# Performance work log

Hardware: AMD Instinct MI355X
Metric: run time of the kernel (lower is better)

The kernel has to match this reference:

```python
import jax, jax.numpy as jnp
import numpy as np

B, S, D, H = 4, 2048, 1024, 16
HD = D // H


def setup_inputs() -> dict:
    key = jax.random.key(0)
    ks = jax.random.split(key, 5)
    s_in = 1.0 / np.sqrt(D)
    return {
        "x": jax.random.normal(ks[0], (B, S, D), dtype=jnp.float32),
        "W_attn": jax.random.uniform(ks[1], (D, 3 * D), dtype=jnp.float32, minval=-s_in, maxval=s_in),
        "b_attn": jax.random.uniform(ks[2], (3 * D,), dtype=jnp.float32, minval=-s_in, maxval=s_in),
        "W_proj": jax.random.uniform(ks[3], (D, D), dtype=jnp.float32, minval=-s_in, maxval=s_in),
        "b_proj": jax.random.uniform(ks[4], (D,), dtype=jnp.float32, minval=-s_in, maxval=s_in),
    }


def reference(x, W_attn, b_attn, W_proj, b_proj):
    b, s, d = x.shape
    qkv = x @ W_attn + b_attn                      # [B,S,3D]
    q, k, v = jnp.split(qkv, 3, axis=-1)
    # [B,H,S,HD]
    q = q.reshape(b, s, H, HD).transpose(0, 2, 1, 3)
    k = k.reshape(b, s, H, HD).transpose(0, 2, 1, 3)
    v = v.reshape(b, s, H, HD).transpose(0, 2, 1, 3)
    scale = 1.0 / np.sqrt(HD)
    att = jnp.einsum("bhqd,bhkd->bhqk", q, k) * scale
    causal = jnp.tril(jnp.ones((s, s), dtype=bool))
    att = jnp.where(causal[None, None], att, -jnp.inf)
    att = jax.nn.softmax(att, axis=-1)
    y = jnp.einsum("bhqk,bhkd->bhqd", att, v)      # [B,H,S,HD]
    y = y.transpose(0, 2, 1, 3).reshape(b, s, d)
    return y @ W_proj + b_proj
```

## Files before the change

kernel.cpp:

```cpp
#include <hip/hip_runtime.h>

#define B_  4
#define S_  2048
#define D_  1024
#define H_  16
#define HD_ 64
#define BS_ (B_*S_)

typedef _Float16 f16;
typedef _Float16 f16_8 __attribute__((ext_vector_type(8)));
typedef _Float16 f16_4 __attribute__((ext_vector_type(4)));
typedef float    f32_4 __attribute__((ext_vector_type(4)));
typedef unsigned int u32;

#define MFMA32(a,b,c) __builtin_amdgcn_mfma_f32_16x16x32_f16(a, b, c, 0, 0, 0)
#define MFMA16(a,b,c) __builtin_amdgcn_mfma_f32_16x16x16f16(a, b, c, 0, 0, 0)
#define NEG_INF (-__builtin_inff())

__device__ inline void gl_lds16(const f16* g, f16* lds_base, int chunk_base) {
    __builtin_amdgcn_global_load_lds(
        (const __attribute__((address_space(1))) u32*)g,
        (__attribute__((address_space(3))) u32*)(lds_base + (size_t)chunk_base * 8),
        16, 0, 0);
}

__global__ __launch_bounds__(256) void x2h(
    const float* __restrict__ X, f16* __restrict__ Xh)
{
    const size_t i = ((size_t)blockIdx.x * 256 + threadIdx.x) * 8;
    float4 a = *(const float4*)&X[i];
    float4 b = *(const float4*)&X[i + 4];
    f16 h[8] = {(f16)a.x,(f16)a.y,(f16)a.z,(f16)a.w,
                (f16)b.x,(f16)b.y,(f16)b.z,(f16)b.w};
    *(uint4*)&Xh[i] = *(const uint4*)h;
}

__global__ __launch_bounds__(256) void trans_w(
    const float* __restrict__ W, f16* __restrict__ Wt, int ncols)
{
    __shared__ f16 T[64][72];
    const int t = threadIdx.x;
    const int n0 = blockIdx.x * 64, k0 = blockIdx.y * 64;
    const int nl4 = (t & 15) * 4;
    #pragma unroll
    for (int r = 0; r < 4; r++) {
        const int kl = (t >> 4) + r * 16;
        float4 v = *(const float4*)&W[(size_t)(k0 + kl) * ncols + n0 + nl4];
        T[nl4 + 0][kl] = (f16)v.x;
        T[nl4 + 1][kl] = (f16)v.y;
        T[nl4 + 2][kl] = (f16)v.z;
        T[nl4 + 3][kl] = (f16)v.w;
    }
    __syncthreads();
    const int nr = t >> 2, kc = (t & 3) * 16;
    *(uint4*)&Wt[(size_t)(n0 + nr) * 1024 + k0 + kc]     = *(uint4*)&T[nr][kc];
    *(uint4*)&Wt[(size_t)(n0 + nr) * 1024 + k0 + kc + 8] = *(uint4*)&T[nr][kc + 8];
}

__global__ __launch_bounds__(256) void qkv_gemm(
    const f16*   __restrict__ Xh,
    const f16*   __restrict__ Wta,
    const float* __restrict__ bias,
    f16* __restrict__ Qb, f16* __restrict__ Kb, f16* __restrict__ Vt)
{
    __shared__ f16 lds[17408];
    f16* Af[2] = {lds,        lds + 4096};
    f16* Bf[2] = {lds + 8192, lds + 12288};
    f16* Ct    = lds;

    const int t    = threadIdx.x;
    const int lane = t & 63;
    const int w    = t >> 6;
    const int quad = lane >> 4, l15 = lane & 15;
    const int wr = w >> 1, wc = w & 1;
    const int n0 = blockIdx.x * 128;
    const int m0 = blockIdx.y * 128;
    const int wbase = t & 192;

    f32_4 acc[4][4] = {};

    for (int k0 = 0; k0 < 1024; k0 += 64) {
        #pragma unroll
        for (int kc = 0; kc < 2; kc++)
            #pragma unroll
            for (int c = 0; c < 2; c++) {
                int i = c*256 + t;
                const int row = i >> 2, col = (i & 3) * 8;
                gl_lds16(Xh  + (size_t)(m0 + row)*1024 + k0 + kc*32 + col,
                         Af[kc], c*256 + wbase);
                gl_lds16(Wta + (size_t)(n0 + row)*1024 + k0 + kc*32 + col,
                         Bf[kc], c*256 + wbase);
            }
        __syncthreads();

        #pragma unroll
        for (int kc = 0; kc < 2; kc++) {
            f16_8 af[4], bf[4];
            #pragma unroll
            for (int mi = 0; mi < 4; mi++)
                af[mi] = *(const f16_8*)&Af[kc][(wr*64 + mi*16 + l15)*32 + quad*8];
            #pragma unroll
            for (int ni = 0; ni < 4; ni++)
                bf[ni] = *(const f16_8*)&Bf[kc][(wc*64 + ni*16 + l15)*32 + quad*8];
            #pragma unroll
            for (int mi = 0; mi < 4; mi++)
                #pragma unroll
                for (int ni = 0; ni < 4; ni++)
                    acc[mi][ni] = MFMA32(af[mi], bf[ni], acc[mi][ni]);
        }
        __syncthreads();
    }

    const int which = n0 >> 10;
    float bcol[4];
    #pragma unroll
    for (int ni = 0; ni < 4; ni++)
        bcol[ni] = bias[n0 + wc*64 + ni*16 + l15];

    if (which < 2) {
        f16* dst = (which == 0) ? Qb : Kb;
        const float sc = (which == 0) ? 0.125f * 1.44269504f : 1.0f;
        #pragma unroll
        for (int mi = 0; mi < 4; mi++)
        #pragma unroll
        for (int ni = 0; ni < 4; ni++)
        #pragma unroll
        for (int r = 0; r < 4; r++) {
            int m = m0 + wr*64 + mi*16 + quad*4 + r;
            int n = (n0 & 1023) + wc*64 + ni*16 + l15;
            int h = n >> 6, hd = n & 63;
            int b = m >> 11, s = m & 2047;
            dst[((size_t)(b*16 + h)*2048 + s)*64 + hd] =
                (f16)((acc[mi][ni][r] + bcol[ni]) * sc);
        }
    } else {
        #pragma unroll
        for (int mi = 0; mi < 4; mi++)
        #pragma unroll
        for (int ni = 0; ni < 4; ni++)
        #pragma unroll
        for (int r = 0; r < 4; r++) {
            int nl = wc*64 + ni*16 + l15;
            int ml = wr*64 + mi*16 + quad*4 + r;
            Ct[nl*136 + ml] = (f16)(acc[mi][ni][r] + bcol[ni]);
        }
        __syncthreads();
        const int row = t >> 1, sc4 = (t & 1) * 64;
        const int n = (n0 & 1023) + row;
        const int h = n >> 6, hd = n & 63;
        const int b = m0 >> 11, s0 = (m0 & 2047) + sc4;
        f16* dst = Vt + ((size_t)(b*16 + h)*64 + hd)*2048 + s0;
        #pragma unroll
        for (int j = 0; j < 8; j++)
            *(uint4*)&dst[j*8] = *(uint4*)&Ct[row*136 + sc4 + j*8];
    }
}

__global__ __launch_bounds__(256) void attn(
    const f16* __restrict__ Qb,
    const f16* __restrict__ Kb,
    const f16* __restrict__ Vt,
    f16* __restrict__ Y)
{
    __shared__ f16 Ks[64*72];
    __shared__ f16 Vs[64*72];

    const int t    = threadIdx.x;
    const int w    = t >> 6;
    const int lane = t & 63;
    const int quad = lane >> 4, l15 = lane & 15;
    const int bh   = blockIdx.y;
    const int b    = bh >> 4, h = bh & 15;

    const f16* qh = Qb + (size_t)bh * S_ * 64;
    const f16* kh = Kb + (size_t)bh * S_ * 64;
    const f16* vt = Vt + (size_t)bh * 64 * S_;

    const int sk = t >> 2, sc = (t & 3) * 8;
    const f16_4 ones = {(f16)1,(f16)1,(f16)1,(f16)1};

    #pragma unroll 1
    for (int sp = 0; sp < 2; sp++) {
        const int qb = sp ? 15 - (int)blockIdx.x : (int)blockIdx.x;
        const int qw = qb*128 + w*32;

        f16_8 qa[2][2];
        #pragma unroll
        for (int rt = 0; rt < 2; rt++)
            #pragma unroll
            for (int c = 0; c < 2; c++)
                qa[rt][c] = *(const f16_8*)&qh[(size_t)(qw + rt*16 + l15)*64 + c*32 + quad*8];

        f32_4 o[2][4] = {};
        f32_4 lacc[2] = {};
        const int ntiles = 2*qb + 2;

        for (int kt = 0; kt < ntiles; kt++) {
            const int kbase = kt * 64;
            *(uint4*)&Ks[sk*72 + sc]      = *(const uint4*)&kh[(size_t)(kbase + sk)*64 + sc];
            *(uint4*)&Ks[sk*72 + sc + 32] = *(const uint4*)&kh[(size_t)(kbase + sk)*64 + sc + 32];
            *(uint4*)&Vs[sk*72 + sc]      = *(const uint4*)&vt[(size_t)sk*2048 + kbase + sc];
            *(uint4*)&Vs[sk*72 + sc + 32] = *(const uint4*)&vt[(size_t)sk*2048 + kbase + sc + 32];
            __syncthreads();

            if (kbase <= qw + 31) {
                f16_8 kb[4][2];
                #pragma unroll
                for (int sub = 0; sub < 4; sub++)
                    #pragma unroll
                    for (int c = 0; c < 2; c++)
                        kb[sub][c] = *(const f16_8*)&Ks[(sub*16 + l15)*72 + c*32 + quad*8];
                f32_4 st[2][4];
                #pragma unroll
                for (int rt = 0; rt < 2; rt++)
                    #pragma unroll
                    for (int sub = 0; sub < 4; sub++) {
                        f32_4 a = {};
                        a = MFMA32(kb[sub][0], qa[rt][0], a);
                        a = MFMA32(kb[sub][1], qa[rt][1], a);
                        st[rt][sub] = a;
                    }

                const bool masked = (kbase + 63 > qw);
                f16_4 pt[2][4];
                #pragma unroll
                for (int rt = 0; rt < 2; rt++)
                #pragma unroll
                for (int sub = 0; sub < 4; sub++) {
                    const int qrow = qw + rt*16 + l15;
                    f16_4 p;
                    #pragma unroll
                    for (int r = 0; r < 4; r++) {
                        float v = st[rt][sub][r];
                        if (masked) {
                            int key = kbase + sub*16 + quad*4 + r;
                            v = (key <= qrow) ? v : NEG_INF;
                        }
                        p[r] = (f16)__builtin_amdgcn_exp2f(v);
                    }
                    pt[rt][sub] = p;
                }

                #pragma unroll
                for (int sub = 0; sub < 4; sub++) {
                    f16_4 vb[4];
                    #pragma unroll
                    for (int tt = 0; tt < 4; tt++)
                        vb[tt] = *(const f16_4*)&Vs[(tt*16 + l15)*72 + sub*16 + quad*4];
                    #pragma unroll
                    for (int rt = 0; rt < 2; rt++) {
                        lacc[rt] = MFMA16(pt[rt][sub], ones, lacc[rt]);
                        #pragma unroll
                        for (int tt = 0; tt < 4; tt++)
                            o[rt][tt] = MFMA16(pt[rt][sub], vb[tt], o[rt][tt]);
                    }
                }
            }
            __syncthreads();
        }

        #pragma unroll
        for (int rt = 0; rt < 2; rt++)
        #pragma unroll
        for (int r = 0; r < 4; r++) {
            float inv = 1.0f / lacc[rt][r];
            int srow = qw + rt*16 + quad*4 + r;
            #pragma unroll
            for (int tt = 0; tt < 4; tt++)
                Y[(size_t)(b*S_ + srow)*1024 + h*64 + tt*16 + l15] =
                    (f16)(o[rt][tt][r] * inv);
        }
    }
}

__global__ __launch_bounds__(256) void proj_gemm(
    const f16* __restrict__ Yb,
    const f16* __restrict__ Wtp,
    const float* __restrict__ bias,
    float* __restrict__ Out)
{
    __shared__ f16 lds2[16384];
    f16* Af[2] = {lds2,        lds2 + 4096};
    f16* Bf[2] = {lds2 + 8192, lds2 + 12288};

    const int t    = threadIdx.x;
    const int lane = t & 63;
    const int w    = t >> 6;
    const int quad = lane >> 4, l15 = lane & 15;
    const int wr = w >> 1, wc = w & 1;
    const int n0 = blockIdx.x * 128;
    const int m0 = blockIdx.y * 128;
    const int wbase = t & 192;

    f32_4 acc[4][4] = {};

    for (int k0 = 0; k0 < 1024; k0 += 64) {
        #pragma unroll
        for (int kc = 0; kc < 2; kc++)
            #pragma unroll
            for (int c = 0; c < 2; c++) {
                int i = c*256 + t;
                const int row = i >> 2, col = (i & 3) * 8;
                gl_lds16(Yb  + (size_t)(m0 + row)*1024 + k0 + kc*32 + col,
                         Af[kc], c*256 + wbase);
                gl_lds16(Wtp + (size_t)(n0 + row)*1024 + k0 + kc*32 + col,
                         Bf[kc], c*256 + wbase);
            }
        __syncthreads();
        #pragma unroll
        for (int kc = 0; kc < 2; kc++) {
            f16_8 af[4], bf[4];
            #pragma unroll
            for (int mi = 0; mi < 4; mi++)
                af[mi] = *(const f16_8*)&Af[kc][(wr*64 + mi*16 + l15)*32 + quad*8];
            #pragma unroll
            for (int ni = 0; ni < 4; ni++)
                bf[ni] = *(const f16_8*)&Bf[kc][(wc*64 + ni*16 + l15)*32 + quad*8];
            #pragma unroll
            for (int mi = 0; mi < 4; mi++)
                #pragma unroll
                for (int ni = 0; ni < 4; ni++)
                    acc[mi][ni] = MFMA32(af[mi], bf[ni], acc[mi][ni]);
        }
        __syncthreads();
    }

    #pragma unroll
    for (int mi = 0; mi < 4; mi++)
    #pragma unroll
    for (int ni = 0; ni < 4; ni++)
    #pragma unroll
    for (int r = 0; r < 4; r++) {
        int m = m0 + wr*64 + mi*16 + quad*4 + r;
        int n = n0 + wc*64 + ni*16 + l15;
        Out[(size_t)m*1024 + n] = acc[mi][ni][r] + bias[n];
    }
}

extern "C" void kernel_launch(void* const* d_in, const int* in_sizes, int n_in,
                              void* d_out, int out_size, void* d_ws, size_t ws_size,
                              hipStream_t stream) {
    const float* x      = (const float*)d_in[0];
    const float* W_attn = (const float*)d_in[1];
    const float* b_attn = (const float*)d_in[2];
    const float* W_proj = (const float*)d_in[3];
    const float* b_proj = (const float*)d_in[4];
    float* out = (float*)d_out;

    const size_t per = (size_t)B_ * H_ * S_ * HD_;
    f16* Yb  = (f16*)d_ws;
    f16* Wta = Yb;
    f16* Qb  = Yb + per;
    f16* Kb  = Qb + per;
    f16* Vt  = Kb + per;
    f16* Wtp = Qb;
    f16* Xh  = (f16*)d_out;

    x2h      <<<BS_*D_/(256*8), 256, 0, stream>>>(x, Xh);
    trans_w  <<<dim3(48, 16), 256, 0, stream>>>(W_attn, Wta, 3*D_);
    qkv_gemm <<<dim3(24, 64), 256, 0, stream>>>(Xh, Wta, b_attn, Qb, Kb, Vt);
    attn     <<<dim3(8, 64),  256, 0, stream>>>(Qb, Kb, Vt, Yb);
    trans_w  <<<dim3(16, 16), 256, 0, stream>>>(W_proj, Wtp, D_);
    proj_gemm<<<dim3(8, 64),  256, 0, stream>>>(Yb, Wtp, b_proj, out);
}
```

Before: 284.8 us.

## Share K/V tiles across paired query blocks in attention; merge prep kernels

The attention kernel now processes its two complementary causal query blocks in one pass over the key/value tiles instead of two sequential passes. Each loaded K/V tile and its fragments in registers are reused by both query blocks, which roughly halves the K/V global loads and LDS reads for the shorter block. In exchange, each thread holds twice the accumulators and query fragments, which raises register pressure and may lower occupancy. Separately, the fp32-to-fp16 conversion of x and the W_attn transpose are merged into one launch to save a kernel launch.

```diff
diff --git a/kernel.cpp b/kernel.cpp
--- a/kernel.cpp
+++ b/kernel.cpp
@@ -24,15 +24,38 @@
         16, 0, 0);
 }
 
-__global__ __launch_bounds__(256) void x2h(
-    const float* __restrict__ X, f16* __restrict__ Xh)
-{
-    const size_t i = ((size_t)blockIdx.x * 256 + threadIdx.x) * 8;
-    float4 a = *(const float4*)&X[i];
-    float4 b = *(const float4*)&X[i + 4];
-    f16 h[8] = {(f16)a.x,(f16)a.y,(f16)a.z,(f16)a.w,
-                (f16)b.x,(f16)b.y,(f16)b.z,(f16)b.w};
-    *(uint4*)&Xh[i] = *(const uint4*)h;
+__global__ __launch_bounds__(256) void prep(
+    const float* __restrict__ X,  f16* __restrict__ Xh,
+    const float* __restrict__ Wa, f16* __restrict__ Wta)
+{
+    __shared__ f16 T[64][72];
+    const int t = threadIdx.x;
+    const int bid = blockIdx.x;
+    if (bid < 4096) {
+        const size_t i = ((size_t)bid * 256 + t) * 8;
+        float4 a = *(const float4*)&X[i];
+        float4 b = *(const float4*)&X[i + 4];
+        f16 h[8] = {(f16)a.x,(f16)a.y,(f16)a.z,(f16)a.w,
+                    (f16)b.x,(f16)b.y,(f16)b.z,(f16)b.w};
+        *(uint4*)&Xh[i] = *(const uint4*)h;
+        return;
+    }
+    const int idx = bid - 4096;
+    const int n0 = (idx % 48) * 64, k0 = (idx / 48) * 64;
+    const int nl4 = (t & 15) * 4;
+    #pragma unroll
+    for (int r = 0; r < 4; r++) {
+        const int kl = (t >> 4) + r * 16;
+        float4 v = *(const float4*)&Wa[(size_t)(k0 + kl) * 3072 + n0 + nl4];
+        T[nl4 + 0][kl] = (f16)v.x;
+        T[nl4 + 1][kl] = (f16)v.y;
+        T[nl4 + 2][kl] = (f16)v.z;
+        T[nl4 + 3][kl] = (f16)v.w;
+    }
+    __syncthreads();
+    const int nr = t >> 2, kc = (t & 3) * 16;
+    *(uint4*)&Wta[(size_t)(n0 + nr) * 1024 + k0 + kc]     = *(uint4*)&T[nr][kc];
+    *(uint4*)&Wta[(size_t)(n0 + nr) * 1024 + k0 + kc + 8] = *(uint4*)&T[nr][kc + 8];
 }
 
 __global__ __launch_bounds__(256) void trans_w(
@@ -179,97 +202,98 @@
     const int sk = t >> 2, sc = (t & 3) * 8;
     const f16_4 ones = {(f16)1,(f16)1,(f16)1,(f16)1};
 
-    #pragma unroll 1
-    for (int sp = 0; sp < 2; sp++) {
-        const int qb = sp ? 15 - (int)blockIdx.x : (int)blockIdx.x;
-        const int qw = qb*128 + w*32;
-
-        f16_8 qa[2][2];
+    const int qb = blockIdx.x;
+    const int qs[2] = {qb*128 + w*32, (15 - qb)*128 + w*32};
+
+    f16_8 qa[2][2][2];
+    #pragma unroll
+    for (int s = 0; s < 2; s++)
         #pragma unroll
         for (int rt = 0; rt < 2; rt++)
             #pragma unroll
             for (int c = 0; c < 2; c++)
-                qa[rt][c] = *(const f16_8*)&qh[(size_t)(qw + rt*16 + l15)*64 + c*32 + quad*8];
-
-        f32_4 o[2][4] = {};
-        f32_4 lacc[2] = {};
-        const int ntiles = 2*qb + 2;
-
-        for (int kt = 0; kt < ntiles; kt++) {
-            const int kbase = kt * 64;
-            *(uint4*)&Ks[sk*72 + sc]      = *(const uint4*)&kh[(size_t)(kbase + sk)*64 + sc];
-            *(uint4*)&Ks[sk*72 + sc + 32] = *(const uint4*)&kh[(size_t)(kbase + sk)*64 + sc + 32];
-            *(uint4*)&Vs[sk*72 + sc]      = *(const uint4*)&vt[(size_t)sk*2048 + kbase + sc];
-            *(uint4*)&Vs[sk*72 + sc + 32] = *(const uint4*)&vt[(size_t)sk*2048 + kbase + sc + 32];
-            __syncthreads();
-
-            if (kbase <= qw + 31) {
-                f16_8 kb[4][2];
+                qa[s][rt][c] = *(const f16_8*)&qh[(size_t)(qs[s] + rt*16 + l15)*64 + c*32 + quad*8];
+
+    f32_4 o[2][2][4] = {};
+    f32_4 lacc[2][2] = {};
+    const int ntiles = 2*(15 - qb) + 2;
+
+    for (int kt = 0; kt < ntiles; kt++) {
+        const int kbase = kt * 64;
+        *(uint4*)&Ks[sk*72 + sc]      = *(const uint4*)&kh[(size_t)(kbase + sk)*64 + sc];
+        *(uint4*)&Ks[sk*72 + sc + 32] = *(const uint4*)&kh[(size_t)(kbase + sk)*64 + sc + 32];
+        *(uint4*)&Vs[sk*72 + sc]      = *(const uint4*)&vt[(size_t)sk*2048 + kbase + sc];
+        *(uint4*)&Vs[sk*72 + sc + 32] = *(const uint4*)&vt[(size_t)sk*2048 + kbase + sc + 32];
+        __syncthreads();
+
+        f16_8 kb[4][2];
+        #pragma unroll
+        for (int sub = 0; sub < 4; sub++)
+            #pragma unroll
+            for (int c = 0; c < 2; c++)
+                kb[sub][c] = *(const f16_8*)&Ks[(sub*16 + l15)*72 + c*32 + quad*8];
+        f16_4 vb[4][4];
+        #pragma unroll
+        for (int sub = 0; sub < 4; sub++)
+            #pragma unroll
+            for (int tt = 0; tt < 4; tt++)
+                vb[sub][tt] = *(const f16_4*)&Vs[(tt*16 + l15)*72 + sub*16 + quad*4];
+
+        #pragma unroll
+        for (int s = 0; s < 2; s++) {
+            if (kbase <= qs[s] + 31) {
+                const bool masked = (kbase + 63 > qs[s]);
                 #pragma unroll
-                for (int sub = 0; sub < 4; sub++)
-                    #pragma unroll
-                    for (int c = 0; c < 2; c++)
-                        kb[sub][c] = *(const f16_8*)&Ks[(sub*16 + l15)*72 + c*32 + quad*8];
-                f32_4 st[2][4];
-                #pragma unroll
-                for (int rt = 0; rt < 2; rt++)
+                for (int rt = 0; rt < 2; rt++) {
+                    f32_4 st[4];
                     #pragma unroll
                     for (int sub = 0; sub < 4; sub++) {
                         f32_4 a = {};
-                        a = MFMA32(kb[sub][0], qa[rt][0], a);
-                        a = MFMA32(kb[sub][1], qa[rt][1], a);
-                        st[rt][sub] = a;
+                        a = MFMA32(kb[sub][0], qa[s][rt][0], a);
+                        a = MFMA32(kb[sub][1], qa[s][rt][1], a);
+                        st[sub] = a;
                     }
-
-                const bool masked = (kbase + 63 > qw);
-                f16_4 pt[2][4];
-                #pragma unroll
-                for (int rt = 0; rt < 2; rt++)
-                #pragma unroll
-                for (int sub = 0; sub < 4; sub++) {
-                    const int qrow = qw + rt*16 + l15;
-                    f16_4 p;
+                    const int qrow = qs[s] + rt*16 + l15;
+                    f16_4 pt[4];
                     #pragma unroll
-                    for (int r = 0; r < 4; r++) {
-                        float v = st[rt][sub][r];
-                        if (masked) {
-                            int key = kbase + sub*16 + quad*4 + r;
-                            v = (key <= qrow) ? v : NEG_INF;
+                    for (int sub = 0; sub < 4; sub++) {
+                        f16_4 p;
+                        #pragma unroll
+                        for (int r = 0; r < 4; r++) {
+                            float x = st[sub][r];
+                            if (masked) {
+                                int key = kbase + sub*16 + quad*4 + r;
+                                x = (key <= qrow) ? x : NEG_INF;
+                            }
+                            p[r] = (f16)__builtin_amdgcn_exp2f(x);
                         }
-                        p[r] = (f16)__builtin_amdgcn_exp2f(v);
+                        pt[sub] = p;
                     }
-                    pt[rt][sub] = p;
-                }
-
-                #pragma unroll
-                for (int sub = 0; sub < 4; sub++) {
-                    f16_4 vb[4];
                     #pragma unroll
-                    for (int tt = 0; tt < 4; tt++)
-                        vb[tt] = *(const f16_4*)&Vs[(tt*16 + l15)*72 + sub*16 + quad*4];
-                    #pragma unroll
-                    for (int rt = 0; rt < 2; rt++) {
-                        lacc[rt] = MFMA16(pt[rt][sub], ones, lacc[rt]);
+                    for (int sub = 0; sub < 4; sub++) {
+                        lacc[s][rt] = MFMA16(pt[sub], ones, lacc[s][rt]);
                         #pragma unroll
                         for (int tt = 0; tt < 4; tt++)
-                            o[rt][tt] = MFMA16(pt[rt][sub], vb[tt], o[rt][tt]);
+                            o[s][rt][tt] = MFMA16(pt[sub], vb[sub][tt], o[s][rt][tt]);
                     }
                 }
             }
-            __syncthreads();
-        }
-
-        #pragma unroll
-        for (int rt = 0; rt < 2; rt++)
-        #pragma unroll
-        for (int r = 0; r < 4; r++) {
-            float inv = 1.0f / lacc[rt][r];
-            int srow = qw + rt*16 + quad*4 + r;
-            #pragma unroll
-            for (int tt = 0; tt < 4; tt++)
-                Y[(size_t)(b*S_ + srow)*1024 + h*64 + tt*16 + l15] =
-                    (f16)(o[rt][tt][r] * inv);
-        }
+        }
+        __syncthreads();
+    }
+
+    #pragma unroll
+    for (int s = 0; s < 2; s++)
+    #pragma unroll
+    for (int rt = 0; rt < 2; rt++)
+    #pragma unroll
+    for (int r = 0; r < 4; r++) {
+        float inv = 1.0f / lacc[s][rt][r];
+        int srow = qs[s] + rt*16 + quad*4 + r;
+        #pragma unroll
+        for (int tt = 0; tt < 4; tt++)
+            Y[(size_t)(b*S_ + srow)*1024 + h*64 + tt*16 + l15] =
+                (f16)(o[s][rt][tt][r] * inv);
     }
 }
 
@@ -356,8 +380,7 @@
     f16* Wtp = Qb;
     f16* Xh  = (f16*)d_out;
 
-    x2h      <<<BS_*D_/(256*8), 256, 0, stream>>>(x, Xh);
-    trans_w  <<<dim3(48, 16), 256, 0, stream>>>(W_attn, Wta, 3*D_);
+    prep     <<<4096 + 768, 256, 0, stream>>>(x, Xh, W_attn, Wta);
     qkv_gemm <<<dim3(24, 64), 256, 0, stream>>>(Xh, Wta, b_attn, Qb, Kb, Vt);
     attn     <<<dim3(8, 64),  256, 0, stream>>>(Qb, Kb, Vt, Yb);
     trans_w  <<<dim3(16, 16), 256, 0, stream>>>(W_proj, Wtp, D_);
```

After: 315.4 us. +10.7%, slower.

## Fuse input conversion with weight transpose and split attention pairs into separate blocks

Applied to the files above, without the earlier changes.

Merges the x-to-fp16 conversion and the W_attn transpose into one launch, removing a kernel launch and its tail. The attention kernel no longer loops over a balanced pair of query blocks per workgroup. It now launches 16x64 blocks, each handling one query block, with heavier blocks scheduled first (qb = 15 - blockIdx.x). This doubles parallelism and relies on the hardware scheduler to balance the causal-triangle work, at the cost of uneven per-block work.

```diff
diff --git a/kernel.cpp b/kernel.cpp
--- a/kernel.cpp
+++ b/kernel.cpp
@@ -24,15 +24,38 @@
         16, 0, 0);
 }
 
-__global__ __launch_bounds__(256) void x2h(
-    const float* __restrict__ X, f16* __restrict__ Xh)
-{
-    const size_t i = ((size_t)blockIdx.x * 256 + threadIdx.x) * 8;
-    float4 a = *(const float4*)&X[i];
-    float4 b = *(const float4*)&X[i + 4];
-    f16 h[8] = {(f16)a.x,(f16)a.y,(f16)a.z,(f16)a.w,
-                (f16)b.x,(f16)b.y,(f16)b.z,(f16)b.w};
-    *(uint4*)&Xh[i] = *(const uint4*)h;
+__global__ __launch_bounds__(256) void prep(
+    const float* __restrict__ X,  f16* __restrict__ Xh,
+    const float* __restrict__ Wa, f16* __restrict__ Wta)
+{
+    __shared__ f16 T[64][72];
+    const int t = threadIdx.x;
+    const int bid = blockIdx.x;
+    if (bid < 4096) {
+        const size_t i = ((size_t)bid * 256 + t) * 8;
+        float4 a = *(const float4*)&X[i];
+        float4 b = *(const float4*)&X[i + 4];
+        f16 h[8] = {(f16)a.x,(f16)a.y,(f16)a.z,(f16)a.w,
+                    (f16)b.x,(f16)b.y,(f16)b.z,(f16)b.w};
+        *(uint4*)&Xh[i] = *(const uint4*)h;
+        return;
+    }
+    const int idx = bid - 4096;
+    const int n0 = (idx % 48) * 64, k0 = (idx / 48) * 64;
+    const int nl4 = (t & 15) * 4;
+    #pragma unroll
+    for (int r = 0; r < 4; r++) {
+        const int kl = (t >> 4) + r * 16;
+        float4 v = *(const float4*)&Wa[(size_t)(k0 + kl) * 3072 + n0 + nl4];
+        T[nl4 + 0][kl] = (f16)v.x;
+        T[nl4 + 1][kl] = (f16)v.y;
+        T[nl4 + 2][kl] = (f16)v.z;
+        T[nl4 + 3][kl] = (f16)v.w;
+    }
+    __syncthreads();
+    const int nr = t >> 2, kc = (t & 3) * 16;
+    *(uint4*)&Wta[(size_t)(n0 + nr) * 1024 + k0 + kc]     = *(uint4*)&T[nr][kc];
+    *(uint4*)&Wta[(size_t)(n0 + nr) * 1024 + k0 + kc + 8] = *(uint4*)&T[nr][kc + 8];
 }
 
 __global__ __launch_bounds__(256) void trans_w(
@@ -179,97 +202,94 @@
     const int sk = t >> 2, sc = (t & 3) * 8;
     const f16_4 ones = {(f16)1,(f16)1,(f16)1,(f16)1};
 
-    #pragma unroll 1
-    for (int sp = 0; sp < 2; sp++) {
-        const int qb = sp ? 15 - (int)blockIdx.x : (int)blockIdx.x;
-        const int qw = qb*128 + w*32;
-
-        f16_8 qa[2][2];
-        #pragma unroll
-        for (int rt = 0; rt < 2; rt++)
-            #pragma unroll
-            for (int c = 0; c < 2; c++)
-                qa[rt][c] = *(const f16_8*)&qh[(size_t)(qw + rt*16 + l15)*64 + c*32 + quad*8];
-
-        f32_4 o[2][4] = {};
-        f32_4 lacc[2] = {};
-        const int ntiles = 2*qb + 2;
-
-        for (int kt = 0; kt < ntiles; kt++) {
-            const int kbase = kt * 64;
-            *(uint4*)&Ks[sk*72 + sc]      = *(const uint4*)&kh[(size_t)(kbase + sk)*64 + sc];
-            *(uint4*)&Ks[sk*72 + sc + 32] = *(const uint4*)&kh[(size_t)(kbase + sk)*64 + sc + 32];
-            *(uint4*)&Vs[sk*72 + sc]      = *(const uint4*)&vt[(size_t)sk*2048 + kbase + sc];
-            *(uint4*)&Vs[sk*72 + sc + 32] = *(const uint4*)&vt[(size_t)sk*2048 + kbase + sc + 32];
-            __syncthreads();
-
-            if (kbase <= qw + 31) {
-                f16_8 kb[4][2];
-                #pragma unroll
-                for (int sub = 0; sub < 4; sub++)
-                    #pragma unroll
-                    for (int c = 0; c < 2; c++)
-                        kb[sub][c] = *(const f16_8*)&Ks[(sub*16 + l15)*72 + c*32 + quad*8];
-                f32_4 st[2][4];
-                #pragma unroll
-                for (int rt = 0; rt < 2; rt++)
-                    #pragma unroll
-                    for (int sub = 0; sub < 4; sub++) {
-                        f32_4 a = {};
-                        a = MFMA32(kb[sub][0], qa[rt][0], a);
-                        a = MFMA32(kb[sub][1], qa[rt][1], a);
-                        st[rt][sub] = a;
+    const int qb = 15 - (int)blockIdx.x;
+    const int qw = qb*128 + w*32;
+
+    f16_8 qa[2][2];
+    #pragma unroll
+    for (int rt = 0; rt < 2; rt++)
+        #pragma unroll
+        for (int c = 0; c < 2; c++)
+            qa[rt][c] = *(const f16_8*)&qh[(size_t)(qw + rt*16 + l15)*64 + c*32 + quad*8];
+
+    f32_4 o[2][4] = {};
+    f32_4 lacc[2] = {};
+    const int ntiles = 2*qb + 2;
+
+    for (int kt = 0; kt < ntiles; kt++) {
+        const int kbase = kt * 64;
+        *(uint4*)&Ks[sk*72 + sc]      = *(const uint4*)&kh[(size_t)(kbase + sk)*64 + sc];
+        *(uint4*)&Ks[sk*72 + sc + 32] = *(const uint4*)&kh[(size_t)(kbase + sk)*64 + sc + 32];
+        *(uint4*)&Vs[sk*72 + sc]      = *(const uint4*)&vt[(size_t)sk*2048 + kbase + sc];
+        *(uint4*)&Vs[sk*72 + sc + 32] = *(const uint4*)&vt[(size_t)sk*2048 + kbase + sc + 32];
+        __syncthreads();
+
+        if (kbase <= qw + 31) {
+            f16_8 kb[4][2];
+            #pragma unroll
+            for (int sub = 0; sub < 4; sub++)
+                #pragma unroll
+                for (int c = 0; c < 2; c++)
+                    kb[sub][c] = *(const f16_8*)&Ks[(sub*16 + l15)*72 + c*32 + quad*8];
+            f32_4 st[2][4];
+            #pragma unroll
+            for (int rt = 0; rt < 2; rt++)
+                #pragma unroll
+                for (int sub = 0; sub < 4; sub++) {
+                    f32_4 a = {};
+                    a = MFMA32(kb[sub][0], qa[rt][0], a);
+                    a = MFMA32(kb[sub][1], qa[rt][1], a);
+                    st[rt][sub] = a;
+                }
+
+            const bool masked = (kbase + 63 > qw);
+            f16_4 pt[2][4];
+            #pragma unroll
+            for (int rt = 0; rt < 2; rt++)
+            #pragma unroll
+            for (int sub = 0; sub < 4; sub++) {
+                const int qrow = qw + rt*16 + l15;
+                f16_4 p;
+                #pragma unroll
+                for (int r = 0; r < 4; r++) {
+                    float x = st[rt][sub][r];
+                    if (masked) {
+                        int key = kbase + sub*16 + quad*4 + r;
+                        x = (key <= qrow) ? x : NEG_INF;
                     }
-
-                const bool masked = (kbase + 63 > qw);
-                f16_4 pt[2][4];
-                #pragma unroll
-                for (int rt = 0; rt < 2; rt++)
-                #pragma unroll
-                for (int sub = 0; sub < 4; sub++) {
-                    const int qrow = qw + rt*16 + l15;
-                    f16_4 p;
-                    #pragma unroll
-                    for (int r = 0; r < 4; r++) {
-                        float v = st[rt][sub][r];
-                        if (masked) {
-                            int key = kbase + sub*16 + quad*4 + r;
-                            v = (key <= qrow) ? v : NEG_INF;
-                        }
-                        p[r] = (f16)__builtin_amdgcn_exp2f(v);
-                    }
-                    pt[rt][sub] = p;
+                    p[r] = (f16)__builtin_amdgcn_exp2f(x);
                 }
-
-                #pragma unroll
-                for (int sub = 0; sub < 4; sub++) {
-                    f16_4 vb[4];
+                pt[rt][sub] = p;
+            }
+
+            #pragma unroll
+            for (int sub = 0; sub < 4; sub++) {
+                f16_4 vb[4];
+                #pragma unroll
+                for (int tt = 0; tt < 4; tt++)
+                    vb[tt] = *(const f16_4*)&Vs[(tt*16 + l15)*72 + sub*16 + quad*4];
+                #pragma unroll
+                for (int rt = 0; rt < 2; rt++) {
+                    lacc[rt] = MFMA16(pt[rt][sub], ones, lacc[rt]);
                     #pragma unroll
                     for (int tt = 0; tt < 4; tt++)
-                        vb[tt] = *(const f16_4*)&Vs[(tt*16 + l15)*72 + sub*16 + quad*4];
-                    #pragma unroll
-                    for (int rt = 0; rt < 2; rt++) {
-                        lacc[rt] = MFMA16(pt[rt][sub], ones, lacc[rt]);
-                        #pragma unroll
-                        for (int tt = 0; tt < 4; tt++)
-                            o[rt][tt] = MFMA16(pt[rt][sub], vb[tt], o[rt][tt]);
-                    }
+                        o[rt][tt] = MFMA16(pt[rt][sub], vb[tt], o[rt][tt]);
                 }
             }
-            __syncthreads();
-        }
-
-        #pragma unroll
-        for (int rt = 0; rt < 2; rt++)
-        #pragma unroll
-        for (int r = 0; r < 4; r++) {
-            float inv = 1.0f / lacc[rt][r];
-            int srow = qw + rt*16 + quad*4 + r;
-            #pragma unroll
-            for (int tt = 0; tt < 4; tt++)
-                Y[(size_t)(b*S_ + srow)*1024 + h*64 + tt*16 + l15] =
-                    (f16)(o[rt][tt][r] * inv);
-        }
+        }
+        __syncthreads();
+    }
+
+    #pragma unroll
+    for (int rt = 0; rt < 2; rt++)
+    #pragma unroll
+    for (int r = 0; r < 4; r++) {
+        float inv = 1.0f / lacc[rt][r];
+        int srow = qw + rt*16 + quad*4 + r;
+        #pragma unroll
+        for (int tt = 0; tt < 4; tt++)
+            Y[(size_t)(b*S_ + srow)*1024 + h*64 + tt*16 + l15] =
+                (f16)(o[rt][tt][r] * inv);
     }
 }
 
@@ -356,10 +376,9 @@
     f16* Wtp = Qb;
     f16* Xh  = (f16*)d_out;
 
-    x2h      <<<BS_*D_/(256*8), 256, 0, stream>>>(x, Xh);
-    trans_w  <<<dim3(48, 16), 256, 0, stream>>>(W_attn, Wta, 3*D_);
+    prep     <<<4096 + 768, 256, 0, stream>>>(x, Xh, W_attn, Wta);
     qkv_gemm <<<dim3(24, 64), 256, 0, stream>>>(Xh, Wta, b_attn, Qb, Kb, Vt);
-    attn     <<<dim3(8, 64),  256, 0, stream>>>(Qb, Kb, Vt, Yb);
+    attn     <<<dim3(16, 64), 256, 0, stream>>>(Qb, Kb, Vt, Yb);
     trans_w  <<<dim3(16, 16), 256, 0, stream>>>(W_proj, Wtp, D_);
     proj_gemm<<<dim3(8, 64),  256, 0, stream>>>(Yb, Wtp, b_proj, out);
 }
```

Result: slower. 335.4 us (+17.8%).
